# Optimization experiments

Measured on AMD Instinct MI355X. Metric: run time of the kernel, lower is better.

## Reference

```python
import jax, jax.numpy as jnp
import numpy as np

B, S, D_IN, D_OUT = 4, 2048, 4096, 4096


def setup_inputs() -> dict:
    key = jax.random.key(0)
    k_x, k_w, k_s, k_b = jax.random.split(key, 4)
    x = jax.random.normal(k_x, (B, S, D_IN), dtype=jnp.float32)
    # ternary weights in {-1, 0, +1}, stored as int (int8 in torch)
    weight_quant = jax.random.randint(k_w, (D_OUT, D_IN), 0, 3, dtype=jnp.int32) - 1
    weight_scale = jax.random.normal(k_s, (D_OUT, 1), dtype=jnp.float32)
    bias = jax.random.normal(k_b, (D_OUT,), dtype=jnp.float32)
    return {"x": x, "weight_quant": weight_quant, "weight_scale": weight_scale, "bias": bias}


def reference(x, weight_quant, weight_scale, bias):
    # dequantize: per-output-row scale applied to ternary weights -> [out, in]
    weight_fp = weight_quant.astype(x.dtype) * weight_scale
    # x @ W^T + b : [B, S, in] x [out, in] -> [B, S, out]
    return jnp.einsum('bsi,oi->bso', x, weight_fp) + bias
```

## Files before the change

kernel.cpp:

```cpp
#include <hip/hip_runtime.h>


#define MDIM 8192
#define NDIM 4096
#define KDIM 4096
#define NT   64

typedef __bf16 bf16x8 __attribute__((ext_vector_type(8)));
typedef float f32x4 __attribute__((ext_vector_type(4)));

#define BAR() asm volatile("s_barrier" ::: "memory")

__device__ __forceinline__ unsigned f2bf_pack(float lo, float hi) {
    unsigned a = __float_as_uint(lo);
    unsigned b = __float_as_uint(hi);
    a += 0x7FFFu + ((a >> 16) & 1u);
    b += 0x7FFFu + ((b >> 16) & 1u);
    return (a >> 16) | (b & 0xFFFF0000u);
}

__device__ __forceinline__ unsigned w2bf_pack(int lo, int hi) {
    unsigned a = __float_as_uint((float)lo) >> 16;
    unsigned b = __float_as_uint((float)hi) & 0xFFFF0000u;
    return a | b;
}

__device__ __forceinline__ void async_load16(const void* gptr, void* lptr) {
    __builtin_amdgcn_global_load_lds(
        (const __attribute__((address_space(1))) void*)gptr,
        (__attribute__((address_space(3))) void*)lptr, 16, 0, 0);
}


#define XG4 ((size_t)MDIM * KDIM / 4)
#define WG4 ((size_t)NDIM * KDIM / 4)
#define CVT_BLOCKS 2048

__global__ __launch_bounds__(256)
void convert_all(const float* __restrict__ X, const int* __restrict__ Wq,
                 uint2* __restrict__ Xb, uint2* __restrict__ Wb) {
    const size_t t0 = (size_t)blockIdx.x * blockDim.x + threadIdx.x;
    const size_t stride = (size_t)gridDim.x * blockDim.x;
#pragma unroll 2
    for (size_t g = t0; g < XG4; g += stride) {
        const f32x4 a = ((const f32x4*)X)[g];
        Xb[g] = make_uint2(f2bf_pack(a.x, a.y), f2bf_pack(a.z, a.w));
    }
#pragma unroll 2
    for (size_t g = t0; g < WG4; g += stride) {
        const int4 a = ((const int4*)Wq)[g];
        Wb[g] = make_uint2(w2bf_pack(a.x, a.y), w2bf_pack(a.z, a.w));
    }
}


#define RDA(b_, P_, mt_, kh_) (*(const bf16x8*)((const char*)As + (b_)*32768 + \
        (P_)*4096 + (mt_)*2048 + ((kh_) ? aB1 : aB0)))
#define RDB(b_, nt_, kh_)     (*(const bf16x8*)((const char*)Bs + (b_)*32768 + \
        (nt_)*2048 + ((kh_) ? bB1 : bB0)))

__global__ __launch_bounds__(512)
void gemm_bf16_8ph(const unsigned short* __restrict__ Xb,
                   const unsigned short* __restrict__ Wb,
                   const float* __restrict__ scale,
                   const float* __restrict__ bias,
                   float* __restrict__ Out) {
    __shared__ unsigned short As[2 * 2 * 128 * 64];
    __shared__ unsigned short Bs[2 * 2 * 128 * 64];

    const int tid  = threadIdx.x;
    const int lane = tid & 63;
    const int wave = tid >> 6;
    const int wm   = wave >> 2;
    const int wn   = wave & 3;
    const int quad = lane >> 4;
    const int l16  = lane & 15;
    const int lr   = lane >> 3;
    const int cc   = (lane & 7) ^ lr;

    int lid = blockIdx.y * 16 + blockIdx.x;
    lid = (lid & 7) * 64 + (lid >> 3);
    const int n0 = (lid & 15) << 8;
    const int m0 = (lid >> 4) << 8;

    const unsigned short* pA[2][2];
    const unsigned short* pB[2][2];
#pragma unroll
    for (int h = 0; h < 2; ++h)
#pragma unroll
        for (int j = 0; j < 2; ++j) {
            pA[h][j] = Xb + (size_t)(m0 + h * 128 + j * 64 + wave * 8 + lr) * KDIM + cc * 8;
            pB[h][j] = Wb + (size_t)(n0 + h * 128 + j * 64 + wave * 8 + lr) * KDIM + cc * 8;
        }

    f32x4 acc[8][4];
#pragma unroll
    for (int i = 0; i < 8; ++i)
#pragma unroll
        for (int j = 0; j < 4; ++j)
            acc[i][j] = (f32x4){0.f, 0.f, 0.f, 0.f};

    const int aoff = l16 * 128 + ((quad ^ (l16 & 7)) << 4);
    const int aB0  = (wm << 14) + aoff;
    const int aB1  = aB0 ^ 64;
    const int bB0  = ((wn >> 1) << 14) + ((wn & 1) << 13) + aoff;
    const int bB1  = bB0 ^ 64;

    auto stageA = [&](int t, int h, int b) {
        char* d = (char*)As + ((b * 2 + h) << 14) + wave * 1024;
        async_load16(pA[h][0] + (size_t)t * 64, d);
        async_load16(pA[h][1] + (size_t)t * 64, d + 8192);
    };
    auto stageB = [&](int t, int h, int b) {
        char* d = (char*)Bs + ((b * 2 + h) << 14) + wave * 1024;
        async_load16(pB[h][0] + (size_t)t * 64, d);
        async_load16(pB[h][1] + (size_t)t * 64, d + 8192);
    };

    auto tile = [&](int t, int b) {
        bf16x8 bfr[4][2];
        {
            bf16x8 af[2][2];
#pragma unroll
            for (int mt = 0; mt < 2; ++mt) {
                af[mt][0] = RDA(b, 0, mt, 0);
                af[mt][1] = RDA(b, 0, mt, 1);
            }
#pragma unroll
            for (int nt = 0; nt < 4; ++nt) {
                bfr[nt][0] = RDB(b, nt, 0);
                bfr[nt][1] = RDB(b, nt, 1);
            }
            if (t + 1 < NT) stageA(t + 1, 0, b ^ 1);
            BAR();
            __builtin_amdgcn_s_setprio(1);
#pragma unroll
            for (int kh = 0; kh < 2; ++kh)
#pragma unroll
                for (int mt = 0; mt < 2; ++mt)
#pragma unroll
                    for (int nt = 0; nt < 4; ++nt)
                        acc[mt][nt] = __builtin_amdgcn_mfma_f32_16x16x32_bf16(
                            af[mt][kh], bfr[nt][kh], acc[mt][nt], 0, 0, 0);
            __builtin_amdgcn_s_setprio(0);
            BAR();
        }
        {
            bf16x8 af[2][2];
#pragma unroll
            for (int mt = 0; mt < 2; ++mt) {
                af[mt][0] = RDA(b, 1, mt, 0);
                af[mt][1] = RDA(b, 1, mt, 1);
            }
            if (t + 1 < NT) stageA(t + 1, 1, b ^ 1);
            BAR();
            __builtin_amdgcn_s_setprio(1);
#pragma unroll
            for (int kh = 0; kh < 2; ++kh)
#pragma unroll
                for (int mt = 0; mt < 2; ++mt)
#pragma unroll
                    for (int nt = 0; nt < 4; ++nt)
                        acc[2 + mt][nt] = __builtin_amdgcn_mfma_f32_16x16x32_bf16(
                            af[mt][kh], bfr[nt][kh], acc[2 + mt][nt], 0, 0, 0);
            __builtin_amdgcn_s_setprio(0);
            BAR();
        }
        {
            bf16x8 af[2][2];
#pragma unroll
            for (int mt = 0; mt < 2; ++mt) {
                af[mt][0] = RDA(b, 2, mt, 0);
                af[mt][1] = RDA(b, 2, mt, 1);
            }
            if (t + 2 < NT) stageB(t + 2, 0, b);
            BAR();
            __builtin_amdgcn_s_setprio(1);
#pragma unroll
            for (int kh = 0; kh < 2; ++kh)
#pragma unroll
                for (int mt = 0; mt < 2; ++mt)
#pragma unroll
                    for (int nt = 0; nt < 4; ++nt)
                        acc[4 + mt][nt] = __builtin_amdgcn_mfma_f32_16x16x32_bf16(
                            af[mt][kh], bfr[nt][kh], acc[4 + mt][nt], 0, 0, 0);
            __builtin_amdgcn_s_setprio(0);
            BAR();
        }
        {
            bf16x8 af[2][2];
#pragma unroll
            for (int mt = 0; mt < 2; ++mt) {
                af[mt][0] = RDA(b, 3, mt, 0);
                af[mt][1] = RDA(b, 3, mt, 1);
            }
            if (t + 2 < NT) stageB(t + 2, 1, b);
            if (t < NT - 2) asm volatile("s_waitcnt vmcnt(4)" ::: "memory");
            else            asm volatile("s_waitcnt vmcnt(0)" ::: "memory");
            BAR();
            __builtin_amdgcn_s_setprio(1);
#pragma unroll
            for (int kh = 0; kh < 2; ++kh)
#pragma unroll
                for (int mt = 0; mt < 2; ++mt)
#pragma unroll
                    for (int nt = 0; nt < 4; ++nt)
                        acc[6 + mt][nt] = __builtin_amdgcn_mfma_f32_16x16x32_bf16(
                            af[mt][kh], bfr[nt][kh], acc[6 + mt][nt], 0, 0, 0);
            __builtin_amdgcn_s_setprio(0);
            BAR();
        }
    };

    stageA(0, 0, 0); stageA(0, 1, 0); stageB(0, 0, 0); stageB(0, 1, 0);
    stageB(1, 0, 1); stageB(1, 1, 1);
    asm volatile("s_waitcnt vmcnt(4)" ::: "memory");
    BAR();

    for (int tt = 0; tt < NT; tt += 2) {
        tile(tt, 0);
        tile(tt + 1, 1);
    }

#pragma unroll
    for (int nt = 0; nt < 4; ++nt) {
        const int n = n0 + wn * 64 + nt * 16 + l16;
        const float sc = scale[n];
        const float bi = bias[n];
#pragma unroll
        for (int mf = 0; mf < 8; ++mf) {
#pragma unroll
            for (int r = 0; r < 4; ++r) {
                const int m = m0 + wm * 128 + mf * 16 + quad * 4 + r;
                Out[(size_t)m * NDIM + n] = acc[mf][nt][r] * sc + bi;
            }
        }
    }
}

#undef RDA
#undef RDB


#define BM 128
#define BN 128
#define BK 64
#define LDSS 72

__global__ __launch_bounds__(256, 2)
void ternary_gemm_fused(const float* __restrict__ X, const int* __restrict__ Wq,
                        const float* __restrict__ scale, const float* __restrict__ bias,
                        float* __restrict__ Out) {
    __shared__ unsigned short As[BM * LDSS];
    __shared__ unsigned short Bs[BN * LDSS];

    const int tid  = threadIdx.x;
    const int lane = tid & 63;
    const int wave = tid >> 6;
    const int quad = lane >> 4;
    const int l16  = lane & 15;
    const int wm   = (wave >> 1) * 64;
    const int wn   = (wave & 1) * 64;

    const int m0 = blockIdx.y * BM;
    const int n0 = blockIdx.x * BN;

    const int srow = tid >> 4;
    const int scol = (tid & 15) * 4;

    const float* Aptr = X  + (size_t)(m0 + srow) * KDIM + scol;
    const int*   Bptr = Wq + (size_t)(n0 + srow) * KDIM + scol;

    f32x4 acc[4][4];
#pragma unroll
    for (int i = 0; i < 4; i++)
#pragma unroll
        for (int j = 0; j < 4; j++)
            acc[i][j] = (f32x4){0.f, 0.f, 0.f, 0.f};

    for (int kt = 0; kt < KDIM; kt += BK) {
        uint2 apk[8], bpk[8];
#pragma unroll
        for (int j = 0; j < 8; j++) {
            const f32x4 av = *(const f32x4*)(Aptr + (size_t)j * 16 * KDIM + kt);
            apk[j].x = f2bf_pack(av.x, av.y);
            apk[j].y = f2bf_pack(av.z, av.w);
        }
#pragma unroll
        for (int j = 0; j < 8; j++) {
            const int4 bv = *(const int4*)(Bptr + (size_t)j * 16 * KDIM + kt);
            bpk[j].x = w2bf_pack(bv.x, bv.y);
            bpk[j].y = w2bf_pack(bv.z, bv.w);
        }
        __syncthreads();
#pragma unroll
        for (int j = 0; j < 8; j++) {
            *(uint2*)&As[(srow + j * 16) * LDSS + scol] = apk[j];
            *(uint2*)&Bs[(srow + j * 16) * LDSS + scol] = bpk[j];
        }
        __syncthreads();

#pragma unroll
        for (int h = 0; h < 2; h++) {
            bf16x8 af[4], bf[4];
#pragma unroll
            for (int mt = 0; mt < 4; mt++)
                af[mt] = *(const bf16x8*)&As[(wm + mt * 16 + l16) * LDSS + h * 32 + quad * 8];
#pragma unroll
            for (int nt = 0; nt < 4; nt++)
                bf[nt] = *(const bf16x8*)&Bs[(wn + nt * 16 + l16) * LDSS + h * 32 + quad * 8];
#pragma unroll
            for (int mt = 0; mt < 4; mt++)
#pragma unroll
                for (int nt = 0; nt < 4; nt++)
                    acc[mt][nt] = __builtin_amdgcn_mfma_f32_16x16x32_bf16(
                        af[mt], bf[nt], acc[mt][nt], 0, 0, 0);
        }
    }

#pragma unroll
    for (int nt = 0; nt < 4; nt++) {
        const int n = n0 + wn + nt * 16 + l16;
        const float sc = scale[n];
        const float bi = bias[n];
#pragma unroll
        for (int mt = 0; mt < 4; mt++) {
#pragma unroll
            for (int r = 0; r < 4; r++) {
                const int m = m0 + wm + mt * 16 + quad * 4 + r;
                Out[(size_t)m * NDIM + n] = acc[mt][nt][r] * sc + bi;
            }
        }
    }
}

extern "C" void kernel_launch(void* const* d_in, const int* in_sizes, int n_in,
                              void* d_out, int out_size, void* d_ws, size_t ws_size,
                              hipStream_t stream) {
    const float* x     = (const float*)d_in[0];
    const int*   wq    = (const int*)d_in[1];
    const float* scale = (const float*)d_in[2];
    const float* bias  = (const float*)d_in[3];
    float* out = (float*)d_out;

    const size_t xb_bytes = (size_t)MDIM * KDIM * 2;
    const size_t wb_bytes = (size_t)NDIM * KDIM * 2;

    if (ws_size >= xb_bytes + wb_bytes) {
        unsigned short* Xb = (unsigned short*)d_ws;
        unsigned short* Wb = (unsigned short*)((char*)d_ws + xb_bytes);

        convert_all<<<CVT_BLOCKS, 256, 0, stream>>>(x, wq, (uint2*)Xb, (uint2*)Wb);

        dim3 grid(NDIM / 256, MDIM / 256);
        gemm_bf16_8ph<<<grid, dim3(512), 0, stream>>>(Xb, Wb, scale, bias, out);
    } else {
        dim3 grid(NDIM / BN, MDIM / BM);
        ternary_gemm_fused<<<grid, dim3(256), 0, stream>>>(x, wq, scale, bias, out);
    }
}
```

Baseline: 508.8 us.

## Triple-buffer A tiles to prefetch two K-steps ahead in bf16 GEMM

```diff
diff --git a/kernel.cpp b/kernel.cpp
--- a/kernel.cpp
+++ b/kernel.cpp
@@ -54,18 +54,13 @@
 }
 
 
-#define RDA(b_, P_, mt_, kh_) (*(const bf16x8*)((const char*)As + (b_)*32768 + \
-        (P_)*4096 + (mt_)*2048 + ((kh_) ? aB1 : aB0)))
-#define RDB(b_, nt_, kh_)     (*(const bf16x8*)((const char*)Bs + (b_)*32768 + \
-        (nt_)*2048 + ((kh_) ? bB1 : bB0)))
-
 __global__ __launch_bounds__(512)
 void gemm_bf16_8ph(const unsigned short* __restrict__ Xb,
                    const unsigned short* __restrict__ Wb,
                    const float* __restrict__ scale,
                    const float* __restrict__ bias,
                    float* __restrict__ Out) {
-    __shared__ unsigned short As[2 * 2 * 128 * 64];
+    __shared__ unsigned short As[3 * 2 * 128 * 64];
     __shared__ unsigned short Bs[2 * 2 * 128 * 64];
 
     const int tid  = threadIdx.x;
@@ -107,31 +102,33 @@
     const int bB1  = bB0 ^ 64;
 
     auto stageA = [&](int t, int h, int b) {
-        char* d = (char*)As + ((b * 2 + h) << 14) + wave * 1024;
+        char* d = (char*)As + b * 32768 + h * 16384 + wave * 1024;
         async_load16(pA[h][0] + (size_t)t * 64, d);
         async_load16(pA[h][1] + (size_t)t * 64, d + 8192);
     };
     auto stageB = [&](int t, int h, int b) {
-        char* d = (char*)Bs + ((b * 2 + h) << 14) + wave * 1024;
+        char* d = (char*)Bs + b * 32768 + h * 16384 + wave * 1024;
         async_load16(pB[h][0] + (size_t)t * 64, d);
         async_load16(pB[h][1] + (size_t)t * 64, d + 8192);
     };
 
-    auto tile = [&](int t, int b) {
+    auto tile = [&](int t, int ab, int bb, int ab2) {
+        const char* Ab = (const char*)As + ab * 32768;
+        const char* Bb = (const char*)Bs + bb * 32768;
         bf16x8 bfr[4][2];
         {
             bf16x8 af[2][2];
 #pragma unroll
             for (int mt = 0; mt < 2; ++mt) {
-                af[mt][0] = RDA(b, 0, mt, 0);
-                af[mt][1] = RDA(b, 0, mt, 1);
+                af[mt][0] = *(const bf16x8*)(Ab + mt * 2048 + aB0);
+                af[mt][1] = *(const bf16x8*)(Ab + mt * 2048 + aB1);
             }
 #pragma unroll
             for (int nt = 0; nt < 4; ++nt) {
-                bfr[nt][0] = RDB(b, nt, 0);
-                bfr[nt][1] = RDB(b, nt, 1);
-            }
-            if (t + 1 < NT) stageA(t + 1, 0, b ^ 1);
+                bfr[nt][0] = *(const bf16x8*)(Bb + nt * 2048 + bB0);
+                bfr[nt][1] = *(const bf16x8*)(Bb + nt * 2048 + bB1);
+            }
+            if (t + 2 < NT) stageA(t + 2, 0, ab2);
             BAR();
             __builtin_amdgcn_s_setprio(1);
 #pragma unroll
@@ -149,10 +146,10 @@
             bf16x8 af[2][2];
 #pragma unroll
             for (int mt = 0; mt < 2; ++mt) {
-                af[mt][0] = RDA(b, 1, mt, 0);
-                af[mt][1] = RDA(b, 1, mt, 1);
-            }
-            if (t + 1 < NT) stageA(t + 1, 1, b ^ 1);
+                af[mt][0] = *(const bf16x8*)(Ab + 4096 + mt * 2048 + aB0);
+                af[mt][1] = *(const bf16x8*)(Ab + 4096 + mt * 2048 + aB1);
+            }
+            if (t + 2 < NT) stageA(t + 2, 1, ab2);
             BAR();
             __builtin_amdgcn_s_setprio(1);
 #pragma unroll
@@ -170,10 +167,10 @@
             bf16x8 af[2][2];
 #pragma unroll
             for (int mt = 0; mt < 2; ++mt) {
-                af[mt][0] = RDA(b, 2, mt, 0);
-                af[mt][1] = RDA(b, 2, mt, 1);
-            }
-            if (t + 2 < NT) stageB(t + 2, 0, b);
+                af[mt][0] = *(const bf16x8*)(Ab + 8192 + mt * 2048 + aB0);
+                af[mt][1] = *(const bf16x8*)(Ab + 8192 + mt * 2048 + aB1);
+            }
+            if (t + 2 < NT) stageB(t + 2, 0, bb);
             BAR();
             __builtin_amdgcn_s_setprio(1);
 #pragma unroll
@@ -191,12 +188,10 @@
             bf16x8 af[2][2];
 #pragma unroll
             for (int mt = 0; mt < 2; ++mt) {
-                af[mt][0] = RDA(b, 3, mt, 0);
-                af[mt][1] = RDA(b, 3, mt, 1);
-            }
-            if (t + 2 < NT) stageB(t + 2, 1, b);
-            if (t < NT - 2) asm volatile("s_waitcnt vmcnt(4)" ::: "memory");
-            else            asm volatile("s_waitcnt vmcnt(0)" ::: "memory");
+                af[mt][0] = *(const bf16x8*)(Ab + 12288 + mt * 2048 + aB0);
+                af[mt][1] = *(const bf16x8*)(Ab + 12288 + mt * 2048 + aB1);
+            }
+            if (t + 2 < NT) stageB(t + 2, 1, bb);
             BAR();
             __builtin_amdgcn_s_setprio(1);
 #pragma unroll
@@ -208,18 +203,23 @@
                         acc[6 + mt][nt] = __builtin_amdgcn_mfma_f32_16x16x32_bf16(
                             af[mt][kh], bfr[nt][kh], acc[6 + mt][nt], 0, 0, 0);
             __builtin_amdgcn_s_setprio(0);
+            if (t < NT - 2) asm volatile("s_waitcnt vmcnt(8)" ::: "memory");
+            else            asm volatile("s_waitcnt vmcnt(0)" ::: "memory");
             BAR();
         }
     };
 
     stageA(0, 0, 0); stageA(0, 1, 0); stageB(0, 0, 0); stageB(0, 1, 0);
-    stageB(1, 0, 1); stageB(1, 1, 1);
-    asm volatile("s_waitcnt vmcnt(4)" ::: "memory");
+    stageA(1, 0, 1); stageA(1, 1, 1); stageB(1, 0, 1); stageB(1, 1, 1);
+    asm volatile("s_waitcnt vmcnt(8)" ::: "memory");
     BAR();
 
-    for (int tt = 0; tt < NT; tt += 2) {
-        tile(tt, 0);
-        tile(tt + 1, 1);
+    int ab = 0;
+    for (int t = 0; t < NT; ++t) {
+        const int bb = t & 1;
+        int ab2 = ab + 2; if (ab2 >= 3) ab2 -= 3;
+        tile(t, ab, bb, ab2);
+        ++ab; if (ab == 3) ab = 0;
     }
 
 #pragma unroll
@@ -237,9 +237,6 @@
         }
     }
 }
-
-#undef RDA
-#undef RDB
 
 
 #define BM 128
```

Result: slower. 539.4 us (+6.0%).

## Prefetch next phase's A fragments from LDS during current MFMA phase

Applied to the files above, without the earlier changes.

```diff
diff --git a/kernel.cpp b/kernel.cpp
--- a/kernel.cpp
+++ b/kernel.cpp
@@ -54,11 +54,6 @@
 }
 
 
-#define RDA(b_, P_, mt_, kh_) (*(const bf16x8*)((const char*)As + (b_)*32768 + \
-        (P_)*4096 + (mt_)*2048 + ((kh_) ? aB1 : aB0)))
-#define RDB(b_, nt_, kh_)     (*(const bf16x8*)((const char*)Bs + (b_)*32768 + \
-        (nt_)*2048 + ((kh_) ? bB1 : bB0)))
-
 __global__ __launch_bounds__(512)
 void gemm_bf16_8ph(const unsigned short* __restrict__ Xb,
                    const unsigned short* __restrict__ Wb,
@@ -106,6 +101,35 @@
     const int bB0  = ((wn >> 1) << 14) + ((wn & 1) << 13) + aoff;
     const int bB1  = bB0 ^ 64;
 
+    bf16x8 afA[2][2], afB[2][2], bfr[4][2];
+
+    auto ldA = [&](bf16x8 dst[2][2], int b, int P) {
+#pragma unroll
+        for (int mt = 0; mt < 2; ++mt) {
+            dst[mt][0] = *(const bf16x8*)((const char*)As + b * 32768 + P * 4096 + mt * 2048 + aB0);
+            dst[mt][1] = *(const bf16x8*)((const char*)As + b * 32768 + P * 4096 + mt * 2048 + aB1);
+        }
+    };
+    auto ldB = [&](int b) {
+#pragma unroll
+        for (int nt = 0; nt < 4; ++nt) {
+            bfr[nt][0] = *(const bf16x8*)((const char*)Bs + b * 32768 + nt * 2048 + bB0);
+            bfr[nt][1] = *(const bf16x8*)((const char*)Bs + b * 32768 + nt * 2048 + bB1);
+        }
+    };
+    auto mfma16 = [&](int q, bf16x8 af[2][2]) {
+        __builtin_amdgcn_s_setprio(1);
+#pragma unroll
+        for (int kh = 0; kh < 2; ++kh)
+#pragma unroll
+            for (int mt = 0; mt < 2; ++mt)
+#pragma unroll
+                for (int nt = 0; nt < 4; ++nt)
+                    acc[q + mt][nt] = __builtin_amdgcn_mfma_f32_16x16x32_bf16(
+                        af[mt][kh], bfr[nt][kh], acc[q + mt][nt], 0, 0, 0);
+        __builtin_amdgcn_s_setprio(0);
+    };
+
     auto stageA = [&](int t, int h, int b) {
         char* d = (char*)As + ((b * 2 + h) << 14) + wave * 1024;
         async_load16(pA[h][0] + (size_t)t * 64, d);
@@ -118,104 +142,36 @@
     };
 
     auto tile = [&](int t, int b) {
-        bf16x8 bfr[4][2];
-        {
-            bf16x8 af[2][2];
-#pragma unroll
-            for (int mt = 0; mt < 2; ++mt) {
-                af[mt][0] = RDA(b, 0, mt, 0);
-                af[mt][1] = RDA(b, 0, mt, 1);
-            }
-#pragma unroll
-            for (int nt = 0; nt < 4; ++nt) {
-                bfr[nt][0] = RDB(b, nt, 0);
-                bfr[nt][1] = RDB(b, nt, 1);
-            }
-            if (t + 1 < NT) stageA(t + 1, 0, b ^ 1);
-            BAR();
-            __builtin_amdgcn_s_setprio(1);
-#pragma unroll
-            for (int kh = 0; kh < 2; ++kh)
-#pragma unroll
-                for (int mt = 0; mt < 2; ++mt)
-#pragma unroll
-                    for (int nt = 0; nt < 4; ++nt)
-                        acc[mt][nt] = __builtin_amdgcn_mfma_f32_16x16x32_bf16(
-                            af[mt][kh], bfr[nt][kh], acc[mt][nt], 0, 0, 0);
-            __builtin_amdgcn_s_setprio(0);
-            BAR();
-        }
-        {
-            bf16x8 af[2][2];
-#pragma unroll
-            for (int mt = 0; mt < 2; ++mt) {
-                af[mt][0] = RDA(b, 1, mt, 0);
-                af[mt][1] = RDA(b, 1, mt, 1);
-            }
-            if (t + 1 < NT) stageA(t + 1, 1, b ^ 1);
-            BAR();
-            __builtin_amdgcn_s_setprio(1);
-#pragma unroll
-            for (int kh = 0; kh < 2; ++kh)
-#pragma unroll
-                for (int mt = 0; mt < 2; ++mt)
-#pragma unroll
-                    for (int nt = 0; nt < 4; ++nt)
-                        acc[2 + mt][nt] = __builtin_amdgcn_mfma_f32_16x16x32_bf16(
-                            af[mt][kh], bfr[nt][kh], acc[2 + mt][nt], 0, 0, 0);
-            __builtin_amdgcn_s_setprio(0);
-            BAR();
-        }
-        {
-            bf16x8 af[2][2];
-#pragma unroll
-            for (int mt = 0; mt < 2; ++mt) {
-                af[mt][0] = RDA(b, 2, mt, 0);
-                af[mt][1] = RDA(b, 2, mt, 1);
-            }
-            if (t + 2 < NT) stageB(t + 2, 0, b);
-            BAR();
-            __builtin_amdgcn_s_setprio(1);
-#pragma unroll
-            for (int kh = 0; kh < 2; ++kh)
-#pragma unroll
-                for (int mt = 0; mt < 2; ++mt)
-#pragma unroll
-                    for (int nt = 0; nt < 4; ++nt)
-                        acc[4 + mt][nt] = __builtin_amdgcn_mfma_f32_16x16x32_bf16(
-                            af[mt][kh], bfr[nt][kh], acc[4 + mt][nt], 0, 0, 0);
-            __builtin_amdgcn_s_setprio(0);
-            BAR();
-        }
-        {
-            bf16x8 af[2][2];
-#pragma unroll
-            for (int mt = 0; mt < 2; ++mt) {
-                af[mt][0] = RDA(b, 3, mt, 0);
-                af[mt][1] = RDA(b, 3, mt, 1);
-            }
-            if (t + 2 < NT) stageB(t + 2, 1, b);
-            if (t < NT - 2) asm volatile("s_waitcnt vmcnt(4)" ::: "memory");
-            else            asm volatile("s_waitcnt vmcnt(0)" ::: "memory");
-            BAR();
-            __builtin_amdgcn_s_setprio(1);
-#pragma unroll
-            for (int kh = 0; kh < 2; ++kh)
-#pragma unroll
-                for (int mt = 0; mt < 2; ++mt)
-#pragma unroll
-                    for (int nt = 0; nt < 4; ++nt)
-                        acc[6 + mt][nt] = __builtin_amdgcn_mfma_f32_16x16x32_bf16(
-                            af[mt][kh], bfr[nt][kh], acc[6 + mt][nt], 0, 0, 0);
-            __builtin_amdgcn_s_setprio(0);
-            BAR();
-        }
+        ldB(b);
+        ldA(afB, b, 1);
+        if (t + 1 < NT) stageA(t + 1, 0, b ^ 1);
+        BAR();
+        mfma16(0, afA);
+        BAR();
+        ldA(afA, b, 2);
+        if (t + 1 < NT) stageA(t + 1, 1, b ^ 1);
+        BAR();
+        mfma16(2, afB);
+        BAR();
+        ldA(afB, b, 3);
+        if (t + 2 < NT) stageB(t + 2, 0, b);
+        BAR();
+        mfma16(4, afA);
+        BAR();
+        if (t + 2 < NT) stageB(t + 2, 1, b);
+        if (t < NT - 2) asm volatile("s_waitcnt vmcnt(4)" ::: "memory");
+        else            asm volatile("s_waitcnt vmcnt(0)" ::: "memory");
+        BAR();
+        if (t + 1 < NT) ldA(afA, b ^ 1, 0);
+        mfma16(6, afB);
+        BAR();
     };
 
     stageA(0, 0, 0); stageA(0, 1, 0); stageB(0, 0, 0); stageB(0, 1, 0);
     stageB(1, 0, 1); stageB(1, 1, 1);
     asm volatile("s_waitcnt vmcnt(4)" ::: "memory");
     BAR();
+    ldA(afA, 0, 0);
 
     for (int tt = 0; tt < NT; tt += 2) {
         tile(tt, 0);
@@ -237,9 +193,6 @@
         }
     }
 }
-
-#undef RDA
-#undef RDB
 
 
 #define BM 128
```

Result: slower. 541.4 us (+6.4%).
